# Optimization experiments

Hardware: AMD Instinct MI355X
Metric: run time of the kernel (lower is better)

## Reference

```python
import jax, jax.numpy as jnp
import numpy as np

BSZ, DIM, SEQ_A, SEQ_B = 16, 768, 1024, 1024


def setup_inputs() -> dict:
    key = jax.random.key(0)
    kA, kB, kU = jax.random.split(key, 3)
    input_A = jax.random.normal(kA, (BSZ, DIM, SEQ_A), dtype=jnp.float32)
    input_B = jax.random.normal(kB, (BSZ, DIM, SEQ_B), dtype=jnp.float32)
    intput_msk = jnp.zeros((BSZ, SEQ_A, SEQ_B), dtype=jnp.float32)  # 0 = on, -inf = off
    U = jax.random.normal(kU, (DIM, DIM), dtype=jnp.float32)
    return {"input_A": input_A, "input_B": input_B, "intput_msk": intput_msk, "U": U}


def reference(input_A, input_B, intput_msk, U):
    # align[b,s,t] = tanh( A[b,:,s]^T U B[b,:,t] )  -> (bsz, seq_A, seq_B)
    align = jnp.einsum("bds,de,bet->bst", input_A, U, input_B)
    align = jnp.tanh(align) + intput_msk
    # per-token scores: max over the other modality's sequence, then softmax
    score_A = jax.nn.softmax(jnp.max(align, axis=2), axis=-1)  # (bsz, seq_A)
    score_B = jax.nn.softmax(jnp.max(align, axis=1), axis=-1)  # (bsz, seq_B)
    output_A = jnp.einsum("bds,bs->bd", input_A, score_A)  # (bsz, dim_A)
    output_B = jnp.einsum("bdt,bt->bd", input_B, score_B)  # (bsz, dim_B)
    return (output_A, output_B)
```

## Files before the change

kernel.cpp:

```cpp
#include <hip/hip_runtime.h>
#include <math.h>

#define BSZ  16
#define DIM  768
#define SEQA 1024
#define SEQB 1024

typedef float f32x4 __attribute__((ext_vector_type(4)));
typedef long long llong;

__device__ inline void gload_lds16(const void* g, void* l) {
    __builtin_amdgcn_global_load_lds(
        (const __attribute__((address_space(1))) void*)g,
        (__attribute__((address_space(3))) void*)l, 16, 0, 0);
}

__device__ inline unsigned enc_key(float f) {
    unsigned u = __float_as_uint(f);
    return (u & 0x80000000u) ? ~u : (u | 0x80000000u);
}
__device__ inline float dec_key(unsigned k) {
    return (k & 0x80000000u) ? __uint_as_float(k ^ 0x80000000u) : __uint_as_float(~k);
}

__device__ inline unsigned pk4_fp8(float a, float b, float c, float d) {
    int v = 0;
    v = __builtin_amdgcn_cvt_pk_fp8_f32(a, b, v, false);
    v = __builtin_amdgcn_cvt_pk_fp8_f32(c, d, v, true);
    return (unsigned)v;
}
__device__ inline unsigned char f2fp8(float a) {
    return (unsigned char)(__builtin_amdgcn_cvt_pk_fp8_f32(a, a, 0, false) & 0xFF);
}

__device__ inline float fast_tanh(float x) {
    float ax = fabsf(x);
    float u = __expf(-2.0f * ax);
    float th = __fdividef(1.0f - u, 1.0f + u);
    return copysignf(th, x);
}

__global__ __launch_bounds__(256) void t_cast_AB(const float* __restrict__ A,
                                                 const float* __restrict__ B,
                                                 unsigned char* __restrict__ At,
                                                 unsigned char* __restrict__ Bt) {
    __shared__ float tl[64][65];
    const int z = blockIdx.z;
    const float* X = (z < BSZ) ? A : B;
    unsigned char* Y = (z < BSZ) ? At : Bt;
    const int b = z & 15;
    const int d0 = blockIdx.y * 64;
    const int s0 = blockIdx.x * 64;
    const int tid = threadIdx.x;
    const int c = tid & 63, r4 = tid >> 6;
    const float* Xb = X + ((size_t)b * DIM + d0) * SEQA + s0;
#pragma unroll
    for (int i = 0; i < 64; i += 4)
        tl[i + r4][c] = Xb[(size_t)(i + r4) * SEQA + c];
    __syncthreads();
    unsigned char* Yb = Y + ((size_t)b * SEQA + s0) * DIM + d0;
    const int m = tid & 15, sl = tid >> 4;
#pragma unroll
    for (int i = 0; i < 4; i++) {
        int s = sl + 16 * i;
        unsigned v = pk4_fp8(tl[4 * m + 0][s], tl[4 * m + 1][s], tl[4 * m + 2][s], tl[4 * m + 3][s]);
        *(unsigned*)&Yb[(size_t)s * DIM + 4 * m] = v;
    }
}

__global__ __launch_bounds__(256) void t_cast_U(const float* __restrict__ U,
                                                unsigned char* __restrict__ Ut,
                                                unsigned* __restrict__ keyA,
                                                unsigned* __restrict__ keyB) {
    __shared__ float tl[64][65];
    const int d0 = blockIdx.y * 64;
    const int e0 = blockIdx.x * 64;
    const int tid = threadIdx.x;
    const int bid = blockIdx.y * gridDim.x + blockIdx.x;
    if (bid < 64) {
        int i = bid * 256 + tid;
        keyA[i] = 0u;
        keyB[i] = 0u;
    }
    const int c = tid & 63, r4 = tid >> 6;
#pragma unroll
    for (int i = 0; i < 64; i += 4)
        tl[i + r4][c] = U[(size_t)(d0 + i + r4) * DIM + e0 + c];
    __syncthreads();
    const int m = tid & 15, sl = tid >> 4;
#pragma unroll
    for (int i = 0; i < 4; i++) {
        int e = sl + 16 * i;
        unsigned v = pk4_fp8(tl[4 * m + 0][e], tl[4 * m + 1][e], tl[4 * m + 2][e], tl[4 * m + 3][e]);
        *(unsigned*)&Ut[(size_t)(e0 + e) * DIM + d0 + 4 * m] = v;
    }
}

__global__ __launch_bounds__(256) void k1_ua(const unsigned char* __restrict__ At,
                                             const unsigned char* __restrict__ Ut,
                                             unsigned char* __restrict__ Ct) {
    __shared__ __align__(16) unsigned char As[2][4096];
    __shared__ __align__(16) unsigned char Us[2][4096];
    const int b  = blockIdx.z;
    const int s0 = blockIdx.x * 128;
    const int e0 = blockIdx.y * 128;
    const int tid = threadIdx.x;
    const int lane = tid & 63;
    const int wid = tid >> 6;
    const int wr = wid >> 1, wc = wid & 1;
    const int quad = lane >> 4, l15 = lane & 15;
    const int grow = lane >> 1, gcol = (lane & 1) * 16;

    const unsigned char* Atb = At + (size_t)b * SEQA * DIM;
    f32x4 acc[4][4] = {};

    for (int d0 = 0; d0 < DIM; d0 += 64) {
#pragma unroll
        for (int h = 0; h < 2; ++h) {
            int db = d0 + 32 * h;
            gload_lds16(Atb + (size_t)(s0 + wid * 32 + grow) * DIM + db + gcol, &As[h][wid * 1024]);
            gload_lds16(Ut  + (size_t)(e0 + wid * 32 + grow) * DIM + db + gcol, &Us[h][wid * 1024]);
        }
        __syncthreads();
#pragma unroll
        for (int h = 0; h < 2; ++h) {
            llong av[4], bv[4];
#pragma unroll
            for (int i = 0; i < 4; ++i)
                av[i] = *(const llong*)&As[h][(wr * 64 + 16 * i + l15) * 32 + quad * 8];
#pragma unroll
            for (int j = 0; j < 4; ++j)
                bv[j] = *(const llong*)&Us[h][(wc * 64 + 16 * j + l15) * 32 + quad * 8];
#pragma unroll
            for (int i = 0; i < 4; ++i)
#pragma unroll
                for (int j = 0; j < 4; ++j)
                    acc[i][j] = __builtin_amdgcn_mfma_f32_16x16x32_fp8_fp8(av[i], bv[j], acc[i][j], 0, 0, 0);
        }
        __syncthreads();
    }
    unsigned char* Cb = Ct + (size_t)b * SEQA * DIM;
#pragma unroll
    for (int i = 0; i < 4; ++i)
#pragma unroll
        for (int j = 0; j < 4; ++j) {
            int e_g = e0 + wc * 64 + 16 * j + l15;
#pragma unroll
            for (int r = 0; r < 4; ++r) {
                int s_g = s0 + wr * 64 + 16 * i + quad * 4 + r;
                Cb[(size_t)s_g * DIM + e_g] = f2fp8(acc[i][j][r]);
            }
        }
}

__global__ __launch_bounds__(256) void k2_align(const unsigned char* __restrict__ Ct,
                                                const unsigned char* __restrict__ Bt,
                                                const float* __restrict__ msk,
                                                unsigned* __restrict__ keyA,
                                                unsigned* __restrict__ keyB) {
    __shared__ __align__(16) unsigned char Cs[2][4096];
    __shared__ __align__(16) unsigned char Bs[2][4096];
    const int b  = blockIdx.z;
    const int t0 = blockIdx.x * 128;
    const int s0 = blockIdx.y * 128;
    const int tid = threadIdx.x;
    const int lane = tid & 63;
    const int wid = tid >> 6;
    const int wr = wid >> 1, wc = wid & 1;
    const int quad = lane >> 4, l15 = lane & 15;
    const int grow = lane >> 1, gcol = (lane & 1) * 16;

    f32x4 acc[4][4] = {};

    for (int e0 = 0; e0 < DIM; e0 += 64) {
#pragma unroll
        for (int h = 0; h < 2; ++h) {
            int eb = e0 + 32 * h;
            gload_lds16(Ct + (size_t)(b * SEQA + s0 + wid * 32 + grow) * DIM + eb + gcol, &Cs[h][wid * 1024]);
            gload_lds16(Bt + (size_t)(b * SEQB + t0 + wid * 32 + grow) * DIM + eb + gcol, &Bs[h][wid * 1024]);
        }
        __syncthreads();
#pragma unroll
        for (int h = 0; h < 2; ++h) {
            llong av[4], bv[4];
#pragma unroll
            for (int i = 0; i < 4; ++i)
                av[i] = *(const llong*)&Cs[h][(wr * 64 + 16 * i + l15) * 32 + quad * 8];
#pragma unroll
            for (int j = 0; j < 4; ++j)
                bv[j] = *(const llong*)&Bs[h][(wc * 64 + 16 * j + l15) * 32 + quad * 8];
#pragma unroll
            for (int i = 0; i < 4; ++i)
#pragma unroll
                for (int j = 0; j < 4; ++j)
                    acc[i][j] = __builtin_amdgcn_mfma_f32_16x16x32_fp8_fp8(av[i], bv[j], acc[i][j], 0, 0, 0);
        }
        __syncthreads();
    }

    const float* Mb = msk + (size_t)b * SEQA * SEQB;
#pragma unroll
    for (int i = 0; i < 4; ++i)
#pragma unroll
        for (int j = 0; j < 4; ++j) {
            int t_g = t0 + wc * 64 + 16 * j + l15;
#pragma unroll
            for (int r = 0; r < 4; ++r) {
                int s_g = s0 + wr * 64 + 16 * i + quad * 4 + r;
                acc[i][j][r] = fast_tanh(acc[i][j][r]) + Mb[(size_t)s_g * SEQB + t_g];
            }
        }
#pragma unroll
    for (int i = 0; i < 4; ++i)
#pragma unroll
        for (int r = 0; r < 4; ++r) {
            float m = fmaxf(fmaxf(acc[i][0][r], acc[i][1][r]), fmaxf(acc[i][2][r], acc[i][3][r]));
            m = fmaxf(m, __shfl_xor(m, 1));
            m = fmaxf(m, __shfl_xor(m, 2));
            m = fmaxf(m, __shfl_xor(m, 4));
            m = fmaxf(m, __shfl_xor(m, 8));
            if (l15 == 0)
                atomicMax(&keyA[b * SEQA + s0 + wr * 64 + 16 * i + quad * 4 + r], enc_key(m));
        }
#pragma unroll
    for (int j = 0; j < 4; ++j) {
        float m = -INFINITY;
#pragma unroll
        for (int i = 0; i < 4; ++i)
#pragma unroll
            for (int r = 0; r < 4; ++r) m = fmaxf(m, acc[i][j][r]);
        m = fmaxf(m, __shfl_xor(m, 16));
        m = fmaxf(m, __shfl_xor(m, 32));
        if (quad == 0)
            atomicMax(&keyB[b * SEQB + t0 + wc * 64 + 16 * j + l15], enc_key(m));
    }
}

__global__ __launch_bounds__(256) void k3_softmax(const unsigned* __restrict__ keyA,
                                                  const unsigned* __restrict__ keyB,
                                                  float* __restrict__ scoreA,
                                                  float* __restrict__ scoreB) {
    const int b = blockIdx.x;
    const bool isA = (blockIdx.y == 0);
    const unsigned* keys = isA ? (keyA + b * SEQA) : (keyB + b * SEQB);
    float* score = isA ? (scoreA + b * SEQA) : (scoreB + b * SEQB);
    __shared__ float sh[4];
    const int tid = threadIdx.x;
    float m[4];
    float mx = -INFINITY;
#pragma unroll
    for (int k = 0; k < 4; k++) {
        m[k] = dec_key(keys[tid + 256 * k]);
        mx = fmaxf(mx, m[k]);
    }
#pragma unroll
    for (int o = 32; o > 0; o >>= 1) mx = fmaxf(mx, __shfl_down(mx, o, 64));
    if ((tid & 63) == 0) sh[tid >> 6] = mx;
    __syncthreads();
    mx = fmaxf(fmaxf(sh[0], sh[1]), fmaxf(sh[2], sh[3]));
    __syncthreads();
    float e[4];
    float sum = 0.f;
#pragma unroll
    for (int k = 0; k < 4; k++) { e[k] = expf(m[k] - mx); sum += e[k]; }
#pragma unroll
    for (int o = 32; o > 0; o >>= 1) sum += __shfl_down(sum, o, 64);
    if ((tid & 63) == 0) sh[tid >> 6] = sum;
    __syncthreads();
    sum = sh[0] + sh[1] + sh[2] + sh[3];
    float inv = 1.0f / sum;
#pragma unroll
    for (int k = 0; k < 4; k++) score[tid + 256 * k] = e[k] * inv;
}

__global__ __launch_bounds__(256) void k4_out(const float* __restrict__ A,
                                              const float* __restrict__ B,
                                              const float* __restrict__ scoreA,
                                              const float* __restrict__ scoreB,
                                              float* __restrict__ out) {
    const int which = blockIdx.y;
    const int row = blockIdx.x * 4 + (threadIdx.x >> 6);
    const int lane = threadIdx.x & 63;
    const float* X = which ? B : A;
    const float* S = which ? scoreB : scoreA;
    const int b = row / DIM;
    const float4* xr = (const float4*)(X + (size_t)row * SEQA);
    const float4* sr = (const float4*)(S + (size_t)b * SEQA);
    float acc = 0.f;
#pragma unroll
    for (int q = lane; q < SEQA / 4; q += 64) {
        float4 x = xr[q];
        float4 s = sr[q];
        acc += x.x * s.x + x.y * s.y + x.z * s.z + x.w * s.w;
    }
#pragma unroll
    for (int o = 32; o > 0; o >>= 1) acc += __shfl_down(acc, o, 64);
    if (lane == 0) out[which * (BSZ * DIM) + row] = acc;
}

extern "C" void kernel_launch(void* const* d_in, const int* in_sizes, int n_in,
                              void* d_out, int out_size, void* d_ws, size_t ws_size,
                              hipStream_t stream) {
    const float* A   = (const float*)d_in[0];
    const float* B   = (const float*)d_in[1];
    const float* msk = (const float*)d_in[2];
    const float* U   = (const float*)d_in[3];
    float* out = (float*)d_out;

    char* ws = (char*)d_ws;
    unsigned char* At = (unsigned char*)ws;
    unsigned char* Bt = (unsigned char*)(ws + 12582912);
    unsigned char* Ct = (unsigned char*)(ws + 25165824);
    unsigned char* Ut = (unsigned char*)(ws + 37748736);
    unsigned* keyA   = (unsigned*)(ws + 38338560);
    unsigned* keyB   = (unsigned*)(ws + 38404096);
    float*    scoreA = (float*)   (ws + 38469632);
    float*    scoreB = (float*)   (ws + 38535168);

    t_cast_U<<<dim3(DIM / 64, DIM / 64, 1), 256, 0, stream>>>(U, Ut, keyA, keyB);
    t_cast_AB<<<dim3(SEQA / 64, DIM / 64, 2 * BSZ), 256, 0, stream>>>(A, B, At, Bt);
    k1_ua<<<dim3(SEQA / 128, DIM / 128, BSZ), 256, 0, stream>>>(At, Ut, Ct);
    k2_align<<<dim3(SEQB / 128, SEQA / 128, BSZ), 256, 0, stream>>>(Ct, Bt, msk, keyA, keyB);
    k3_softmax<<<dim3(BSZ, 2), 256, 0, stream>>>(keyA, keyB, scoreA, scoreB);
    k4_out<<<dim3(BSZ * DIM / 4, 2), 256, 0, stream>>>(A, B, scoreA, scoreB, out);
}
```

Before: 259.8 us.

## Swizzle LDS layout, swap MFMA operands for packed stores, reorder k2 grid

New measurement: 257.1 us. About the same (-1.1%).

```diff
diff --git a/kernel.cpp b/kernel.cpp
--- a/kernel.cpp
+++ b/kernel.cpp
@@ -28,9 +28,6 @@
     v = __builtin_amdgcn_cvt_pk_fp8_f32(a, b, v, false);
     v = __builtin_amdgcn_cvt_pk_fp8_f32(c, d, v, true);
     return (unsigned)v;
-}
-__device__ inline unsigned char f2fp8(float a) {
-    return (unsigned char)(__builtin_amdgcn_cvt_pk_fp8_f32(a, a, 0, false) & 0xFF);
 }
 
 __device__ inline float fast_tanh(float x) {
@@ -109,7 +106,9 @@
     const int wid = tid >> 6;
     const int wr = wid >> 1, wc = wid & 1;
     const int quad = lane >> 4, l15 = lane & 15;
-    const int grow = lane >> 1, gcol = (lane & 1) * 16;
+    const int grow = lane >> 1;
+    const int gcol = ((lane & 1) ^ ((lane >> 3) & 1)) * 16;
+    const int koff = (((quad >> 1) ^ ((l15 >> 2) & 1)) << 4) + (quad & 1) * 8;
 
     const unsigned char* Atb = At + (size_t)b * SEQA * DIM;
     f32x4 acc[4][4] = {};
@@ -127,10 +126,10 @@
             llong av[4], bv[4];
 #pragma unroll
             for (int i = 0; i < 4; ++i)
-                av[i] = *(const llong*)&As[h][(wr * 64 + 16 * i + l15) * 32 + quad * 8];
+                av[i] = *(const llong*)&Us[h][(wr * 64 + 16 * i + l15) * 32 + koff];
 #pragma unroll
             for (int j = 0; j < 4; ++j)
-                bv[j] = *(const llong*)&Us[h][(wc * 64 + 16 * j + l15) * 32 + quad * 8];
+                bv[j] = *(const llong*)&As[h][(wc * 64 + 16 * j + l15) * 32 + koff];
 #pragma unroll
             for (int i = 0; i < 4; ++i)
 #pragma unroll
@@ -144,12 +143,10 @@
     for (int i = 0; i < 4; ++i)
 #pragma unroll
         for (int j = 0; j < 4; ++j) {
-            int e_g = e0 + wc * 64 + 16 * j + l15;
-#pragma unroll
-            for (int r = 0; r < 4; ++r) {
-                int s_g = s0 + wr * 64 + 16 * i + quad * 4 + r;
-                Cb[(size_t)s_g * DIM + e_g] = f2fp8(acc[i][j][r]);
-            }
+            int e_g = e0 + wr * 64 + 16 * i + quad * 4;
+            int s_g = s0 + wc * 64 + 16 * j + l15;
+            unsigned v = pk4_fp8(acc[i][j][0], acc[i][j][1], acc[i][j][2], acc[i][j][3]);
+            *(unsigned*)&Cb[(size_t)s_g * DIM + e_g] = v;
         }
 }
 
@@ -160,15 +157,17 @@
                                                 unsigned* __restrict__ keyB) {
     __shared__ __align__(16) unsigned char Cs[2][4096];
     __shared__ __align__(16) unsigned char Bs[2][4096];
-    const int b  = blockIdx.z;
-    const int t0 = blockIdx.x * 128;
-    const int s0 = blockIdx.y * 128;
+    const int b  = blockIdx.x;
+    const int t0 = blockIdx.y * 128;
+    const int s0 = blockIdx.z * 128;
     const int tid = threadIdx.x;
     const int lane = tid & 63;
     const int wid = tid >> 6;
     const int wr = wid >> 1, wc = wid & 1;
     const int quad = lane >> 4, l15 = lane & 15;
-    const int grow = lane >> 1, gcol = (lane & 1) * 16;
+    const int grow = lane >> 1;
+    const int gcol = ((lane & 1) ^ ((lane >> 3) & 1)) * 16;
+    const int koff = (((quad >> 1) ^ ((l15 >> 2) & 1)) << 4) + (quad & 1) * 8;
 
     f32x4 acc[4][4] = {};
 
@@ -185,10 +184,10 @@
             llong av[4], bv[4];
 #pragma unroll
             for (int i = 0; i < 4; ++i)
-                av[i] = *(const llong*)&Cs[h][(wr * 64 + 16 * i + l15) * 32 + quad * 8];
+                av[i] = *(const llong*)&Bs[h][(wr * 64 + 16 * i + l15) * 32 + koff];
 #pragma unroll
             for (int j = 0; j < 4; ++j)
-                bv[j] = *(const llong*)&Bs[h][(wc * 64 + 16 * j + l15) * 32 + quad * 8];
+                bv[j] = *(const llong*)&Cs[h][(wc * 64 + 16 * j + l15) * 32 + koff];
 #pragma unroll
             for (int i = 0; i < 4; ++i)
 #pragma unroll
@@ -203,13 +202,26 @@
     for (int i = 0; i < 4; ++i)
 #pragma unroll
         for (int j = 0; j < 4; ++j) {
-            int t_g = t0 + wc * 64 + 16 * j + l15;
-#pragma unroll
-            for (int r = 0; r < 4; ++r) {
-                int s_g = s0 + wr * 64 + 16 * i + quad * 4 + r;
-                acc[i][j][r] = fast_tanh(acc[i][j][r]) + Mb[(size_t)s_g * SEQB + t_g];
-            }
-        }
+            int s_g = s0 + wc * 64 + 16 * j + l15;
+            int t_g = t0 + wr * 64 + 16 * i + quad * 4;
+            float4 mv = *(const float4*)&Mb[(size_t)s_g * SEQB + t_g];
+            acc[i][j][0] = fast_tanh(acc[i][j][0]) + mv.x;
+            acc[i][j][1] = fast_tanh(acc[i][j][1]) + mv.y;
+            acc[i][j][2] = fast_tanh(acc[i][j][2]) + mv.z;
+            acc[i][j][3] = fast_tanh(acc[i][j][3]) + mv.w;
+        }
+#pragma unroll
+    for (int j = 0; j < 4; ++j) {
+        float m = -INFINITY;
+#pragma unroll
+        for (int i = 0; i < 4; ++i)
+#pragma unroll
+            for (int r = 0; r < 4; ++r) m = fmaxf(m, acc[i][j][r]);
+        m = fmaxf(m, __shfl_xor(m, 16));
+        m = fmaxf(m, __shfl_xor(m, 32));
+        if (quad == 0)
+            atomicMax(&keyA[b * SEQA + s0 + wc * 64 + 16 * j + l15], enc_key(m));
+    }
 #pragma unroll
     for (int i = 0; i < 4; ++i)
 #pragma unroll
@@ -220,20 +232,8 @@
             m = fmaxf(m, __shfl_xor(m, 4));
             m = fmaxf(m, __shfl_xor(m, 8));
             if (l15 == 0)
-                atomicMax(&keyA[b * SEQA + s0 + wr * 64 + 16 * i + quad * 4 + r], enc_key(m));
-        }
-#pragma unroll
-    for (int j = 0; j < 4; ++j) {
-        float m = -INFINITY;
-#pragma unroll
-        for (int i = 0; i < 4; ++i)
-#pragma unroll
-            for (int r = 0; r < 4; ++r) m = fmaxf(m, acc[i][j][r]);
-        m = fmaxf(m, __shfl_xor(m, 16));
-        m = fmaxf(m, __shfl_xor(m, 32));
-        if (quad == 0)
-            atomicMax(&keyB[b * SEQB + t0 + wc * 64 + 16 * j + l15], enc_key(m));
-    }
+                atomicMax(&keyB[b * SEQB + t0 + wr * 64 + 16 * i + quad * 4 + r], enc_key(m));
+        }
 }
 
 __global__ __launch_bounds__(256) void k3_softmax(const unsigned* __restrict__ keyA,
@@ -320,7 +320,7 @@
     t_cast_U<<<dim3(DIM / 64, DIM / 64, 1), 256, 0, stream>>>(U, Ut, keyA, keyB);
     t_cast_AB<<<dim3(SEQA / 64, DIM / 64, 2 * BSZ), 256, 0, stream>>>(A, B, At, Bt);
     k1_ua<<<dim3(SEQA / 128, DIM / 128, BSZ), 256, 0, stream>>>(At, Ut, Ct);
-    k2_align<<<dim3(SEQB / 128, SEQA / 128, BSZ), 256, 0, stream>>>(Ct, Bt, msk, keyA, keyB);
+    k2_align<<<dim3(BSZ, SEQB / 128, SEQA / 128), 256, 0, stream>>>(Ct, Bt, msk, keyA, keyB);
     k3_softmax<<<dim3(BSZ, 2), 256, 0, stream>>>(keyA, keyB, scoreA, scoreB);
     k4_out<<<dim3(BSZ * DIM / 4, 2), 256, 0, stream>>>(A, B, scoreA, scoreB, out);
 }
```

## Deepen GEMM K-tiles with swizzled LDS, vectorize transposes, prefetch mask early

Applied to the files above, without the earlier changes.

Result: faster. 245.9 us (-5.4%).

```diff
diff --git a/kernel.cpp b/kernel.cpp
--- a/kernel.cpp
+++ b/kernel.cpp
@@ -44,7 +44,7 @@
                                                  const float* __restrict__ B,
                                                  unsigned char* __restrict__ At,
                                                  unsigned char* __restrict__ Bt) {
-    __shared__ float tl[64][65];
+    __shared__ float tl[64][68];
     const int z = blockIdx.z;
     const float* X = (z < BSZ) ? A : B;
     unsigned char* Y = (z < BSZ) ? At : Bt;
@@ -52,11 +52,14 @@
     const int d0 = blockIdx.y * 64;
     const int s0 = blockIdx.x * 64;
     const int tid = threadIdx.x;
-    const int c = tid & 63, r4 = tid >> 6;
+    const int rr = tid >> 4, c4 = tid & 15;
     const float* Xb = X + ((size_t)b * DIM + d0) * SEQA + s0;
 #pragma unroll
-    for (int i = 0; i < 64; i += 4)
-        tl[i + r4][c] = Xb[(size_t)(i + r4) * SEQA + c];
+    for (int i = 0; i < 4; i++) {
+        int row = i * 16 + rr;
+        float4 v = *(const float4*)&Xb[(size_t)row * SEQA + c4 * 4];
+        *(float4*)&tl[row][c4 * 4] = v;
+    }
     __syncthreads();
     unsigned char* Yb = Y + ((size_t)b * SEQA + s0) * DIM + d0;
     const int m = tid & 15, sl = tid >> 4;
@@ -72,7 +75,7 @@
                                                 unsigned char* __restrict__ Ut,
                                                 unsigned* __restrict__ keyA,
                                                 unsigned* __restrict__ keyB) {
-    __shared__ float tl[64][65];
+    __shared__ float tl[64][68];
     const int d0 = blockIdx.y * 64;
     const int e0 = blockIdx.x * 64;
     const int tid = threadIdx.x;
@@ -82,10 +85,13 @@
         keyA[i] = 0u;
         keyB[i] = 0u;
     }
-    const int c = tid & 63, r4 = tid >> 6;
-#pragma unroll
-    for (int i = 0; i < 64; i += 4)
-        tl[i + r4][c] = U[(size_t)(d0 + i + r4) * DIM + e0 + c];
+    const int rr = tid >> 4, c4 = tid & 15;
+#pragma unroll
+    for (int i = 0; i < 4; i++) {
+        int row = i * 16 + rr;
+        float4 v = *(const float4*)&U[(size_t)(d0 + row) * DIM + e0 + c4 * 4];
+        *(float4*)&tl[row][c4 * 4] = v;
+    }
     __syncthreads();
     const int m = tid & 15, sl = tid >> 4;
 #pragma unroll
@@ -96,11 +102,31 @@
     }
 }
 
+__device__ inline void stage_tile(const unsigned char* __restrict__ src, int row0,
+                                  int kbyte0, unsigned char* lds, int wid, int lane) {
+    const int r8 = lane >> 3;
+    const int g  = lane & 7;
+    const int gg = g ^ (r8 & 7);
+#pragma unroll
+    for (int t = 0; t < 4; ++t) {
+        int row = row0 + wid * 32 + t * 8 + r8;
+        gload_lds16(src + (size_t)row * DIM + kbyte0 + gg * 16,
+                    lds + (wid * 32 + t * 8) * 128 + lane * 16);
+    }
+}
+
+__device__ inline llong frag_read(const unsigned char* lds, int rowbase, int l15,
+                                  int quad, int h) {
+    int gg = 2 * h + (quad >> 1);
+    int off = (rowbase + l15) * 128 + ((gg ^ (l15 & 7)) << 4) + (quad & 1) * 8;
+    return *(const llong*)(lds + off);
+}
+
 __global__ __launch_bounds__(256) void k1_ua(const unsigned char* __restrict__ At,
                                              const unsigned char* __restrict__ Ut,
                                              unsigned char* __restrict__ Ct) {
-    __shared__ __align__(16) unsigned char As[2][4096];
-    __shared__ __align__(16) unsigned char Us[2][4096];
+    __shared__ __align__(16) unsigned char As[128 * 128];
+    __shared__ __align__(16) unsigned char Us[128 * 128];
     const int b  = blockIdx.z;
     const int s0 = blockIdx.x * 128;
     const int e0 = blockIdx.y * 128;
@@ -109,28 +135,21 @@
     const int wid = tid >> 6;
     const int wr = wid >> 1, wc = wid & 1;
     const int quad = lane >> 4, l15 = lane & 15;
-    const int grow = lane >> 1, gcol = (lane & 1) * 16;
 
     const unsigned char* Atb = At + (size_t)b * SEQA * DIM;
     f32x4 acc[4][4] = {};
 
-    for (int d0 = 0; d0 < DIM; d0 += 64) {
-#pragma unroll
-        for (int h = 0; h < 2; ++h) {
-            int db = d0 + 32 * h;
-            gload_lds16(Atb + (size_t)(s0 + wid * 32 + grow) * DIM + db + gcol, &As[h][wid * 1024]);
-            gload_lds16(Ut  + (size_t)(e0 + wid * 32 + grow) * DIM + db + gcol, &Us[h][wid * 1024]);
-        }
+    for (int d0 = 0; d0 < DIM; d0 += 128) {
+        stage_tile(Atb + (size_t)s0 * DIM, 0, d0, As, wid, lane);
+        stage_tile(Ut + (size_t)e0 * DIM, 0, d0, Us, wid, lane);
         __syncthreads();
 #pragma unroll
-        for (int h = 0; h < 2; ++h) {
+        for (int h = 0; h < 4; ++h) {
             llong av[4], bv[4];
 #pragma unroll
-            for (int i = 0; i < 4; ++i)
-                av[i] = *(const llong*)&As[h][(wr * 64 + 16 * i + l15) * 32 + quad * 8];
-#pragma unroll
-            for (int j = 0; j < 4; ++j)
-                bv[j] = *(const llong*)&Us[h][(wc * 64 + 16 * j + l15) * 32 + quad * 8];
+            for (int i = 0; i < 4; ++i) av[i] = frag_read(As, wr * 64 + 16 * i, l15, quad, h);
+#pragma unroll
+            for (int j = 0; j < 4; ++j) bv[j] = frag_read(Us, wc * 64 + 16 * j, l15, quad, h);
 #pragma unroll
             for (int i = 0; i < 4; ++i)
 #pragma unroll
@@ -153,13 +172,13 @@
         }
 }
 
-__global__ __launch_bounds__(256) void k2_align(const unsigned char* __restrict__ Ct,
-                                                const unsigned char* __restrict__ Bt,
-                                                const float* __restrict__ msk,
-                                                unsigned* __restrict__ keyA,
-                                                unsigned* __restrict__ keyB) {
-    __shared__ __align__(16) unsigned char Cs[2][4096];
-    __shared__ __align__(16) unsigned char Bs[2][4096];
+__global__ __launch_bounds__(256, 2) void k2_align(const unsigned char* __restrict__ Ct,
+                                                   const unsigned char* __restrict__ Bt,
+                                                   const float* __restrict__ msk,
+                                                   unsigned* __restrict__ keyA,
+                                                   unsigned* __restrict__ keyB) {
+    __shared__ __align__(16) unsigned char Cs[128 * 128];
+    __shared__ __align__(16) unsigned char Bs[128 * 128];
     const int b  = blockIdx.z;
     const int t0 = blockIdx.x * 128;
     const int s0 = blockIdx.y * 128;
@@ -168,27 +187,31 @@
     const int wid = tid >> 6;
     const int wr = wid >> 1, wc = wid & 1;
     const int quad = lane >> 4, l15 = lane & 15;
-    const int grow = lane >> 1, gcol = (lane & 1) * 16;
+
+    const float* Mb = msk + (size_t)b * SEQA * SEQB;
+    float4 mv[4][4];
+#pragma unroll
+    for (int i = 0; i < 4; ++i)
+#pragma unroll
+        for (int j = 0; j < 4; ++j) {
+            int s_g = s0 + wc * 64 + 16 * j + l15;
+            int t_g = t0 + wr * 64 + 16 * i + quad * 4;
+            mv[i][j] = *(const float4*)&Mb[(size_t)s_g * SEQB + t_g];
+        }
 
     f32x4 acc[4][4] = {};
 
-    for (int e0 = 0; e0 < DIM; e0 += 64) {
-#pragma unroll
-        for (int h = 0; h < 2; ++h) {
-            int eb = e0 + 32 * h;
-            gload_lds16(Ct + (size_t)(b * SEQA + s0 + wid * 32 + grow) * DIM + eb + gcol, &Cs[h][wid * 1024]);
-            gload_lds16(Bt + (size_t)(b * SEQB + t0 + wid * 32 + grow) * DIM + eb + gcol, &Bs[h][wid * 1024]);
-        }
+    for (int e0 = 0; e0 < DIM; e0 += 128) {
+        stage_tile(Ct + (size_t)(b * SEQA + s0) * DIM, 0, e0, Cs, wid, lane);
+        stage_tile(Bt + (size_t)(b * SEQB + t0) * DIM, 0, e0, Bs, wid, lane);
         __syncthreads();
 #pragma unroll
-        for (int h = 0; h < 2; ++h) {
+        for (int h = 0; h < 4; ++h) {
             llong av[4], bv[4];
 #pragma unroll
-            for (int i = 0; i < 4; ++i)
-                av[i] = *(const llong*)&Cs[h][(wr * 64 + 16 * i + l15) * 32 + quad * 8];
-#pragma unroll
-            for (int j = 0; j < 4; ++j)
-                bv[j] = *(const llong*)&Bs[h][(wc * 64 + 16 * j + l15) * 32 + quad * 8];
+            for (int i = 0; i < 4; ++i) av[i] = frag_read(Bs, wr * 64 + 16 * i, l15, quad, h);
+#pragma unroll
+            for (int j = 0; j < 4; ++j) bv[j] = frag_read(Cs, wc * 64 + 16 * j, l15, quad, h);
 #pragma unroll
             for (int i = 0; i < 4; ++i)
 #pragma unroll
@@ -198,18 +221,27 @@
         __syncthreads();
     }
 
-    const float* Mb = msk + (size_t)b * SEQA * SEQB;
 #pragma unroll
     for (int i = 0; i < 4; ++i)
 #pragma unroll
         for (int j = 0; j < 4; ++j) {
-            int t_g = t0 + wc * 64 + 16 * j + l15;
-#pragma unroll
-            for (int r = 0; r < 4; ++r) {
-                int s_g = s0 + wr * 64 + 16 * i + quad * 4 + r;
-                acc[i][j][r] = fast_tanh(acc[i][j][r]) + Mb[(size_t)s_g * SEQB + t_g];
-            }
-        }
+            acc[i][j][0] = fast_tanh(acc[i][j][0]) + mv[i][j].x;
+            acc[i][j][1] = fast_tanh(acc[i][j][1]) + mv[i][j].y;
+            acc[i][j][2] = fast_tanh(acc[i][j][2]) + mv[i][j].z;
+            acc[i][j][3] = fast_tanh(acc[i][j][3]) + mv[i][j].w;
+        }
+#pragma unroll
+    for (int j = 0; j < 4; ++j) {
+        float m = -INFINITY;
+#pragma unroll
+        for (int i = 0; i < 4; ++i)
+#pragma unroll
+            for (int r = 0; r < 4; ++r) m = fmaxf(m, acc[i][j][r]);
+        m = fmaxf(m, __shfl_xor(m, 16));
+        m = fmaxf(m, __shfl_xor(m, 32));
+        if (quad == 0)
+            atomicMax(&keyA[b * SEQA + s0 + wc * 64 + 16 * j + l15], enc_key(m));
+    }
 #pragma unroll
     for (int i = 0; i < 4; ++i)
 #pragma unroll
@@ -220,20 +252,8 @@
             m = fmaxf(m, __shfl_xor(m, 4));
             m = fmaxf(m, __shfl_xor(m, 8));
             if (l15 == 0)
-                atomicMax(&keyA[b * SEQA + s0 + wr * 64 + 16 * i + quad * 4 + r], enc_key(m));
-        }
-#pragma unroll
-    for (int j = 0; j < 4; ++j) {
-        float m = -INFINITY;
-#pragma unroll
-        for (int i = 0; i < 4; ++i)
-#pragma unroll
-            for (int r = 0; r < 4; ++r) m = fmaxf(m, acc[i][j][r]);
-        m = fmaxf(m, __shfl_xor(m, 16));
-        m = fmaxf(m, __shfl_xor(m, 32));
-        if (quad == 0)
-            atomicMax(&keyB[b * SEQB + t0 + wc * 64 + 16 * j + l15], enc_key(m));
-    }
+                atomicMax(&keyB[b * SEQB + t0 + wr * 64 + 16 * i + quad * 4 + r], enc_key(m));
+        }
 }
 
 __global__ __launch_bounds__(256) void k3_softmax(const unsigned* __restrict__ keyA,
```

## Fuse fp32-to-fp8 transpose-cast of A and B into GEMM operand staging

Applied to the files above, without the earlier changes.

Result: slower. 277.3 us (+6.7%).

```diff
diff --git a/kernel.cpp b/kernel.cpp
--- a/kernel.cpp
+++ b/kernel.cpp
@@ -8,6 +8,7 @@
 
 typedef float f32x4 __attribute__((ext_vector_type(4)));
 typedef long long llong;
+typedef unsigned long long ullong;
 
 __device__ inline void gload_lds16(const void* g, void* l) {
     __builtin_amdgcn_global_load_lds(
@@ -40,39 +41,11 @@
     return copysignf(th, x);
 }
 
-__global__ __launch_bounds__(256) void t_cast_AB(const float* __restrict__ A,
-                                                 const float* __restrict__ B,
-                                                 unsigned char* __restrict__ At,
-                                                 unsigned char* __restrict__ Bt) {
-    __shared__ float tl[64][65];
-    const int z = blockIdx.z;
-    const float* X = (z < BSZ) ? A : B;
-    unsigned char* Y = (z < BSZ) ? At : Bt;
-    const int b = z & 15;
-    const int d0 = blockIdx.y * 64;
-    const int s0 = blockIdx.x * 64;
-    const int tid = threadIdx.x;
-    const int c = tid & 63, r4 = tid >> 6;
-    const float* Xb = X + ((size_t)b * DIM + d0) * SEQA + s0;
-#pragma unroll
-    for (int i = 0; i < 64; i += 4)
-        tl[i + r4][c] = Xb[(size_t)(i + r4) * SEQA + c];
-    __syncthreads();
-    unsigned char* Yb = Y + ((size_t)b * SEQA + s0) * DIM + d0;
-    const int m = tid & 15, sl = tid >> 4;
-#pragma unroll
-    for (int i = 0; i < 4; i++) {
-        int s = sl + 16 * i;
-        unsigned v = pk4_fp8(tl[4 * m + 0][s], tl[4 * m + 1][s], tl[4 * m + 2][s], tl[4 * m + 3][s]);
-        *(unsigned*)&Yb[(size_t)s * DIM + 4 * m] = v;
-    }
-}
-
 __global__ __launch_bounds__(256) void t_cast_U(const float* __restrict__ U,
                                                 unsigned char* __restrict__ Ut,
                                                 unsigned* __restrict__ keyA,
                                                 unsigned* __restrict__ keyB) {
-    __shared__ float tl[64][65];
+    __shared__ float tl[64][68];
     const int d0 = blockIdx.y * 64;
     const int e0 = blockIdx.x * 64;
     const int tid = threadIdx.x;
@@ -82,10 +55,13 @@
         keyA[i] = 0u;
         keyB[i] = 0u;
     }
-    const int c = tid & 63, r4 = tid >> 6;
-#pragma unroll
-    for (int i = 0; i < 64; i += 4)
-        tl[i + r4][c] = U[(size_t)(d0 + i + r4) * DIM + e0 + c];
+    const int rr = tid >> 4, c4 = tid & 15;
+#pragma unroll
+    for (int i = 0; i < 4; i++) {
+        int row = i * 16 + rr;
+        float4 v = *(const float4*)&U[(size_t)(d0 + row) * DIM + e0 + c4 * 4];
+        *(float4*)&tl[row][c4 * 4] = v;
+    }
     __syncthreads();
     const int m = tid & 15, sl = tid >> 4;
 #pragma unroll
@@ -96,99 +72,68 @@
     }
 }
 
-__global__ __launch_bounds__(256) void k1_ua(const unsigned char* __restrict__ At,
+__device__ inline void stage_rows64(const unsigned char* __restrict__ src, int kbyte0,
+                                    unsigned char* lds, int wid, int lane) {
+#pragma unroll
+    for (int t = 0; t < 2; ++t) {
+        int row = wid * 32 + t * 16 + (lane >> 2);
+        int sg = (lane & 3) ^ (row & 3);
+        gload_lds16(src + (size_t)row * DIM + kbyte0 + sg * 16,
+                    lds + wid * 2048 + t * 1024 + lane * 16);
+    }
+}
+__device__ inline llong frag_rows64(const unsigned char* lds, int rr, int g, int half) {
+    return *(const llong*)(lds + rr * 64 + ((g ^ (rr & 3)) << 4) + half * 8);
+}
+
+__device__ inline void stage_cast64(const float* __restrict__ X, int k0, int n0,
+                                    unsigned char* lds, int wid, int lane) {
+    const int nl = wid * 32 + (lane & 31);
+    const int c8b = lane >> 5;
+#pragma unroll
+    for (int t = 0; t < 4; ++t) {
+        int c8 = c8b + 2 * t;
+        const float* g = X + (size_t)(k0 + c8 * 8) * SEQA + n0 + nl;
+        float v0 = g[0 * SEQA], v1 = g[1 * SEQA], v2 = g[2 * SEQA], v3 = g[3 * SEQA];
+        float v4 = g[4 * SEQA], v5 = g[5 * SEQA], v6 = g[6 * SEQA], v7 = g[7 * SEQA];
+        ullong w = (ullong)pk4_fp8(v0, v1, v2, v3) | ((ullong)pk4_fp8(v4, v5, v6, v7) << 32);
+        *(ullong*)(lds + nl * 64 + ((c8 ^ (nl & 7)) << 3)) = w;
+    }
+}
+__device__ inline llong frag_cast64(const unsigned char* lds, int rr, int s8) {
+    return *(const llong*)(lds + rr * 64 + ((s8 ^ (rr & 7)) << 3));
+}
+
+__global__ __launch_bounds__(256) void k1_ua(const float* __restrict__ A,
                                              const unsigned char* __restrict__ Ut,
                                              unsigned char* __restrict__ Ct) {
-    __shared__ __align__(16) unsigned char As[2][4096];
-    __shared__ __align__(16) unsigned char Us[2][4096];
+    __shared__ __align__(16) unsigned char Asw[128 * 64];
+    __shared__ __align__(16) unsigned char Us[128 * 64];
     const int b  = blockIdx.z;
-    const int s0 = blockIdx.x * 128;
-    const int e0 = blockIdx.y * 128;
-    const int tid = threadIdx.x;
-    const int lane = tid & 63;
-    const int wid = tid >> 6;
-    const int wr = wid >> 1, wc = wid & 1;
-    const int quad = lane >> 4, l15 = lane & 15;
-    const int grow = lane >> 1, gcol = (lane & 1) * 16;
-
-    const unsigned char* Atb = At + (size_t)b * SEQA * DIM;
-    f32x4 acc[4][4] = {};
-
-    for (int d0 = 0; d0 < DIM; d0 += 64) {
-#pragma unroll
-        for (int h = 0; h < 2; ++h) {
-            int db = d0 + 32 * h;
-            gload_lds16(Atb + (size_t)(s0 + wid * 32 + grow) * DIM + db + gcol, &As[h][wid * 1024]);
-            gload_lds16(Ut  + (size_t)(e0 + wid * 32 + grow) * DIM + db + gcol, &Us[h][wid * 1024]);
-        }
-        __syncthreads();
-#pragma unroll
-        for (int h = 0; h < 2; ++h) {
-            llong av[4], bv[4];
-#pragma unroll
-            for (int i = 0; i < 4; ++i)
-                av[i] = *(const llong*)&As[h][(wr * 64 + 16 * i + l15) * 32 + quad * 8];
-#pragma unroll
-            for (int j = 0; j < 4; ++j)
-                bv[j] = *(const llong*)&Us[h][(wc * 64 + 16 * j + l15) * 32 + quad * 8];
-#pragma unroll
-            for (int i = 0; i < 4; ++i)
-#pragma unroll
-                for (int j = 0; j < 4; ++j)
-                    acc[i][j] = __builtin_amdgcn_mfma_f32_16x16x32_fp8_fp8(av[i], bv[j], acc[i][j], 0, 0, 0);
-        }
-        __syncthreads();
-    }
-    unsigned char* Cb = Ct + (size_t)b * SEQA * DIM;
-#pragma unroll
-    for (int i = 0; i < 4; ++i)
-#pragma unroll
-        for (int j = 0; j < 4; ++j) {
-            int e_g = e0 + wc * 64 + 16 * j + l15;
-#pragma unroll
-            for (int r = 0; r < 4; ++r) {
-                int s_g = s0 + wr * 64 + 16 * i + quad * 4 + r;
-                Cb[(size_t)s_g * DIM + e_g] = f2fp8(acc[i][j][r]);
-            }
-        }
-}
-
-__global__ __launch_bounds__(256) void k2_align(const unsigned char* __restrict__ Ct,
-                                                const unsigned char* __restrict__ Bt,
-                                                const float* __restrict__ msk,
-                                                unsigned* __restrict__ keyA,
-                                                unsigned* __restrict__ keyB) {
-    __shared__ __align__(16) unsigned char Cs[2][4096];
-    __shared__ __align__(16) unsigned char Bs[2][4096];
-    const int b  = blockIdx.z;
-    const int t0 = blockIdx.x * 128;
+    const int e0 = blockIdx.x * 128;
     const int s0 = blockIdx.y * 128;
     const int tid = threadIdx.x;
     const int lane = tid & 63;
     const int wid = tid >> 6;
     const int wr = wid >> 1, wc = wid & 1;
     const int quad = lane >> 4, l15 = lane & 15;
-    const int grow = lane >> 1, gcol = (lane & 1) * 16;
-
+
+    const float* Ab = A + (size_t)b * DIM * SEQA;
     f32x4 acc[4][4] = {};
 
-    for (int e0 = 0; e0 < DIM; e0 += 64) {
-#pragma unroll
-        for (int h = 0; h < 2; ++h) {
-            int eb = e0 + 32 * h;
-            gload_lds16(Ct + (size_t)(b * SEQA + s0 + wid * 32 + grow) * DIM + eb + gcol, &Cs[h][wid * 1024]);
-            gload_lds16(Bt + (size_t)(b * SEQB + t0 + wid * 32 + grow) * DIM + eb + gcol, &Bs[h][wid * 1024]);
-        }
+    for (int d0 = 0; d0 < DIM; d0 += 64) {
+        stage_rows64(Ut + (size_t)e0 * DIM, d0, Us, wid, lane);
+        stage_cast64(Ab, d0, s0, Asw, wid, lane);
         __syncthreads();
 #pragma unroll
         for (int h = 0; h < 2; ++h) {
             llong av[4], bv[4];
 #pragma unroll
             for (int i = 0; i < 4; ++i)
-                av[i] = *(const llong*)&Cs[h][(wr * 64 + 16 * i + l15) * 32 + quad * 8];
+                av[i] = frag_cast64(Asw, wr * 64 + 16 * i + l15, h * 4 + quad);
 #pragma unroll
             for (int j = 0; j < 4; ++j)
-                bv[j] = *(const llong*)&Bs[h][(wc * 64 + 16 * j + l15) * 32 + quad * 8];
+                bv[j] = frag_rows64(Us, wc * 64 + 16 * j + l15, h * 2 + (quad >> 1), quad & 1);
 #pragma unroll
             for (int i = 0; i < 4; ++i)
 #pragma unroll
@@ -197,19 +142,86 @@
         }
         __syncthreads();
     }
-
-    const float* Mb = msk + (size_t)b * SEQA * SEQB;
+    unsigned char* Cb = Ct + (size_t)b * SEQA * DIM;
 #pragma unroll
     for (int i = 0; i < 4; ++i)
 #pragma unroll
         for (int j = 0; j < 4; ++j) {
-            int t_g = t0 + wc * 64 + 16 * j + l15;
+            int e_g = e0 + wc * 64 + 16 * j + l15;
 #pragma unroll
             for (int r = 0; r < 4; ++r) {
                 int s_g = s0 + wr * 64 + 16 * i + quad * 4 + r;
-                acc[i][j][r] = fast_tanh(acc[i][j][r]) + Mb[(size_t)s_g * SEQB + t_g];
+                Cb[(size_t)s_g * DIM + e_g] = f2fp8(acc[i][j][r]);
             }
         }
+}
+
+__global__ __launch_bounds__(256) void k2_align(const unsigned char* __restrict__ Ct,
+                                                const float* __restrict__ B,
+                                                const float* __restrict__ msk,
+                                                unsigned* __restrict__ keyA,
+                                                unsigned* __restrict__ keyB) {
+    __shared__ __align__(16) unsigned char Bsw[128 * 64];
+    __shared__ __align__(16) unsigned char Cs[128 * 64];
+    const int b  = blockIdx.z;
+    const int s0 = blockIdx.x * 128;
+    const int t0 = blockIdx.y * 128;
+    const int tid = threadIdx.x;
+    const int lane = tid & 63;
+    const int wid = tid >> 6;
+    const int wr = wid >> 1, wc = wid & 1;
+    const int quad = lane >> 4, l15 = lane & 15;
+
+    const float* Bb = B + (size_t)b * DIM * SEQB;
+    f32x4 acc[4][4] = {};
+
+    for (int e0k = 0; e0k < DIM; e0k += 64) {
+        stage_rows64(Ct + (size_t)(b * SEQA + s0) * DIM, e0k, Cs, wid, lane);
+        stage_cast64(Bb, e0k, t0, Bsw, wid, lane);
+        __syncthreads();
+#pragma unroll
+        for (int h = 0; h < 2; ++h) {
+            llong av[4], bv[4];
+#pragma unroll
+            for (int i = 0; i < 4; ++i)
+                av[i] = frag_cast64(Bsw, wr * 64 + 16 * i + l15, h * 4 + quad);
+#pragma unroll
+            for (int j = 0; j < 4; ++j)
+                bv[j] = frag_rows64(Cs, wc * 64 + 16 * j + l15, h * 2 + (quad >> 1), quad & 1);
+#pragma unroll
+            for (int i = 0; i < 4; ++i)
+#pragma unroll
+                for (int j = 0; j < 4; ++j)
+                    acc[i][j] = __builtin_amdgcn_mfma_f32_16x16x32_fp8_fp8(av[i], bv[j], acc[i][j], 0, 0, 0);
+        }
+        __syncthreads();
+    }
+
+    const float* Mb = msk + (size_t)b * SEQA * SEQB;
+#pragma unroll
+    for (int i = 0; i < 4; ++i)
+#pragma unroll
+        for (int j = 0; j < 4; ++j) {
+            int s_g = s0 + wc * 64 + 16 * j + l15;
+            int t_g = t0 + wr * 64 + 16 * i + quad * 4;
+            float4 mv = *(const float4*)&Mb[(size_t)s_g * SEQB + t_g];
+            acc[i][j][0] = fast_tanh(acc[i][j][0]) + mv.x;
+            acc[i][j][1] = fast_tanh(acc[i][j][1]) + mv.y;
+            acc[i][j][2] = fast_tanh(acc[i][j][2]) + mv.z;
+            acc[i][j][3] = fast_tanh(acc[i][j][3]) + mv.w;
+        }
+#pragma unroll
+    for (int j = 0; j < 4; ++j) {
+        float m = -INFINITY;
+#pragma unroll
+        for (int i = 0; i < 4; ++i)
+#pragma unroll
+            for (int r = 0; r < 4; ++r) m = fmaxf(m, acc[i][j][r]);
+        m = fmaxf(m, __shfl_xor(m, 16));
+        m = fmaxf(m, __shfl_xor(m, 32));
+        if (quad == 0)
+            atomicMax(&keyA[b * SEQA + s0 + wc * 64 + 16 * j + l15], enc_key(m));
+    }
 #pragma unroll
     for (int i = 0; i < 4; ++i)
 #pragma unroll
@@ -220,20 +232,8 @@
             m = fmaxf(m, __shfl_xor(m, 4));
             m = fmaxf(m, __shfl_xor(m, 8));
             if (l15 == 0)
-                atomicMax(&keyA[b * SEQA + s0 + wr * 64 + 16 * i + quad * 4 + r], enc_key(m));
-        }
-#pragma unroll
-    for (int j = 0; j < 4; ++j) {
-        float m = -INFINITY;
-#pragma unroll
-        for (int i = 0; i < 4; ++i)
-#pragma unroll
-            for (int r = 0; r < 4; ++r) m = fmaxf(m, acc[i][j][r]);
-        m = fmaxf(m, __shfl_xor(m, 16));
-        m = fmaxf(m, __shfl_xor(m, 32));
-        if (quad == 0)
-            atomicMax(&keyB[b * SEQB + t0 + wc * 64 + 16 * j + l15], enc_key(m));
-    }
+                atomicMax(&keyB[b * SEQB + t0 + wr * 64 + 16 * i + quad * 4 + r], enc_key(m));
+        }
 }
 
 __global__ __launch_bounds__(256) void k3_softmax(const unsigned* __restrict__ keyA,
@@ -308,19 +308,16 @@
     float* out = (float*)d_out;
 
     char* ws = (char*)d_ws;
-    unsigned char* At = (unsigned char*)ws;
-    unsigned char* Bt = (unsigned char*)(ws + 12582912);
-    unsigned char* Ct = (unsigned char*)(ws + 25165824);
-    unsigned char* Ut = (unsigned char*)(ws + 37748736);
-    unsigned* keyA   = (unsigned*)(ws + 38338560);
-    unsigned* keyB   = (unsigned*)(ws + 38404096);
-    float*    scoreA = (float*)   (ws + 38469632);
-    float*    scoreB = (float*)   (ws + 38535168);
+    unsigned char* Ct = (unsigned char*)ws;
+    unsigned char* Ut = (unsigned char*)(ws + 12582912);
+    unsigned* keyA   = (unsigned*)(ws + 13172736);
+    unsigned* keyB   = (unsigned*)(ws + 13238272);
+    float*    scoreA = (float*)   (ws + 13303808);
+    float*    scoreB = (float*)   (ws + 13369344);
 
     t_cast_U<<<dim3(DIM / 64, DIM / 64, 1), 256, 0, stream>>>(U, Ut, keyA, keyB);
-    t_cast_AB<<<dim3(SEQA / 64, DIM / 64, 2 * BSZ), 256, 0, stream>>>(A, B, At, Bt);
-    k1_ua<<<dim3(SEQA / 128, DIM / 128, BSZ), 256, 0, stream>>>(At, Ut, Ct);
-    k2_align<<<dim3(SEQB / 128, SEQA / 128, BSZ), 256, 0, stream>>>(Ct, Bt, msk, keyA, keyB);
+    k1_ua<<<dim3(DIM / 128, SEQA / 128, BSZ), 256, 0, stream>>>(A, Ut, Ct);
+    k2_align<<<dim3(SEQA / 128, SEQB / 128, BSZ), 256, 0, stream>>>(Ct, B, msk, keyA, keyB);
     k3_softmax<<<dim3(BSZ, 2), 256, 0, stream>>>(keyA, keyB, scoreA, scoreB);
     k4_out<<<dim3(BSZ * DIM / 4, 2), 256, 0, stream>>>(A, B, scoreA, scoreB, out);
 }
```
